# Kernel optimization log

Measured on AMD Instinct MI355X. Metric: run time of the kernel, lower is better.

The kernel has to match this reference:

```python
import jax, jax.numpy as jnp
import numpy as np

N = 20000
E = 320000
IN_DIM = 128
HID = 64
HEADS = 8
OUT_DIM = 128
NEG_SLOPE = 0.2  # PyG GATConv default leaky_relu slope


def _glorot(key, shape):
    fan_in = shape[0] if len(shape) > 1 else shape[-1]
    return jax.random.normal(key, shape, dtype=jnp.float32) / jnp.sqrt(jnp.float32(fan_in))


def setup_inputs() -> dict:
    key = jax.random.key(0)
    ks = jax.random.split(key, 16)
    x = jax.random.normal(ks[0], (N, IN_DIM), dtype=jnp.float32)
    edge_index = jax.random.randint(ks[1], (2, E), 0, N, dtype=jnp.int32)
    HC = HEADS * HID
    return {
        "x": x,
        "edge_index": edge_index,
        # layer 1: in -> heads*hid (concat)
        "W1": _glorot(ks[2], (IN_DIM, HC)),
        "a_src1": _glorot(ks[3], (HEADS, HID)),
        "a_dst1": _glorot(ks[4], (HEADS, HID)),
        "b1": jnp.zeros((HC,), jnp.float32),
        # layer 2: heads*hid -> heads*hid (concat)
        "W2": _glorot(ks[5], (HC, HC)),
        "a_src2": _glorot(ks[6], (HEADS, HID)),
        "a_dst2": _glorot(ks[7], (HEADS, HID)),
        "b2": jnp.zeros((HC,), jnp.float32),
        # layer 3: heads*hid -> out, heads=1, concat=False
        "W3": _glorot(ks[8], (HC, OUT_DIM)),
        "a_src3": _glorot(ks[9], (1, OUT_DIM)),
        "a_dst3": _glorot(ks[10], (1, OUT_DIM)),
        "b3": jnp.zeros((OUT_DIM,), jnp.float32),
    }


def _gat_layer(x, src, dst, W, a_src, a_dst, b, heads, concat):
    # x: [N, F_in] -> h: [N, H, C]
    n = x.shape[0]
    h = (x @ W).reshape(n, heads, -1)
    # per-node attention half-logits: [N, H]
    al_src = jnp.sum(h * a_src[None], axis=-1)
    al_dst = jnp.sum(h * a_dst[None], axis=-1)
    # per-edge logits with leaky relu: [E, H]
    e = jax.nn.leaky_relu(al_src[src] + al_dst[dst], NEG_SLOPE)
    # segment softmax over incoming edges of each dst node
    emax = jax.ops.segment_max(e, dst, num_segments=n)
    ex = jnp.exp(e - emax[dst])
    den = jax.ops.segment_sum(ex, dst, num_segments=n)
    alpha = ex / (den[dst] + 1e-16)
    # weighted scatter-aggregate of source features: [E, H, C] -> [N, H, C]
    out = jax.ops.segment_sum(h[src] * alpha[:, :, None], dst, num_segments=n)
    out = out.reshape(n, -1) if concat else out.mean(axis=1)
    return out + b


def reference(x, edge_index, W1, a_src1, a_dst1, b1, W2, a_src2, a_dst2, b2,
              W3, a_src3, a_dst3, b3):
    # PyG GATConv adds self-loops by default
    loops = jnp.arange(N, dtype=edge_index.dtype)
    src = jnp.concatenate([edge_index[0], loops])
    dst = jnp.concatenate([edge_index[1], loops])
    # eval mode: dropout is identity
    h = _gat_layer(x, src, dst, W1, a_src1, a_dst1, b1, HEADS, True)
    h = jax.nn.elu(h)
    h = _gat_layer(h, src, dst, W2, a_src2, a_dst2, b2, HEADS, True)
    h = jax.nn.elu(h)
    out = _gat_layer(h, src, dst, W3, a_src3, a_dst3, b3, 1, False)
    return out
```

## Files before the change

### kernel.cpp

```cpp
#include <hip/hip_runtime.h>
#include <math.h>

#define NN 20000
#define EE 320000
#define ETOT 340000
#define NHEADS 8
#define HID 64
#define HCV 512
#define IND 128
#define OUTD 128
#define NEG_SLOPE 0.2f
#define LOG2E 1.4426950408889634f

typedef __attribute__((ext_vector_type(8))) _Float16 half8;
typedef __attribute__((ext_vector_type(4))) _Float16 half4;
typedef __attribute__((ext_vector_type(4))) float floatx4;

#define S1 (IND * HCV)
#define S2 (HCV * HCV)
#define S3 (HCV * OUTD)
#define XTOT (NN * IND)

#define NT1 64
#define NT2 320
#define NT_TOT 384
#define XB 2500
__global__ __launch_bounds__(256) void prep_kernel(const float* __restrict__ W1,
                                                   const float* __restrict__ W2,
                                                   const float* __restrict__ W3,
                                                   const float* __restrict__ x,
                                                   _Float16* __restrict__ T1,
                                                   _Float16* __restrict__ T2,
                                                   _Float16* __restrict__ T3,
                                                   _Float16* __restrict__ xh,
                                                   int* __restrict__ cnt) {
    int b = blockIdx.x;
    int tid = threadIdx.x;
    if (b < NT_TOT) {
        __shared__ _Float16 tile[32][34];
        const float* W; _Float16* T; int K, N, tb;
        if (b < NT1)      { W = W1; T = T1; K = IND; N = HCV;  tb = b; }
        else if (b < NT2) { W = W2; T = T2; K = HCV; N = HCV;  tb = b - NT1; }
        else              { W = W3; T = T3; K = HCV; N = OUTD; tb = b - NT2; }
        int ntn = N >> 5;
        int k0 = (tb / ntn) * 32, n0 = (tb % ntn) * 32;
        int tx = tid & 31, ty0 = tid >> 5;
        #pragma unroll
        for (int i = 0; i < 4; i++) {
            int ty = ty0 + 8 * i;
            tile[ty][tx] = (_Float16)W[(size_t)(k0 + ty) * N + n0 + tx];
        }
        __syncthreads();
        #pragma unroll
        for (int i = 0; i < 4; i++) {
            int ty = ty0 + 8 * i;
            T[(size_t)(n0 + ty) * K + k0 + tx] = tile[tx][ty];
        }
    } else if (b < NT_TOT + XB) {
        int idx = (b - NT_TOT) * 256 + tid;
        int j = idx * 4;
        float4 v = *(const float4*)&x[j];
        half4 o;
        o[0] = (_Float16)v.x; o[1] = (_Float16)v.y;
        o[2] = (_Float16)v.z; o[3] = (_Float16)v.w;
        *(half4*)&xh[j] = o;
    } else {
        int idx = (b - NT_TOT - XB) * 256 + tid;
        if (idx < NN) cnt[idx] = 0;
    }
}


__global__ void count_kernel(const int* __restrict__ ei, int* __restrict__ cnt) {
    int i = blockIdx.x * blockDim.x + threadIdx.x;
    if (i >= ETOT) return;
    int v = (i < EE) ? ei[EE + i] : (i - EE);
    atomicAdd(&cnt[v], 1);
}

#define SCH 20
__global__ __launch_bounds__(1024) void scan_kernel(const int* __restrict__ cnt,
                                                    int* __restrict__ row_ptr,
                                                    int* __restrict__ cursor) {
    __shared__ int wtot[16];
    __shared__ int woff[16];
    int t = threadIdx.x;
    int lane = t & 63;
    int wid = t >> 6;
    int base = t * SCH;
    int vals[SCH];
    int s = 0;
    #pragma unroll
    for (int i = 0; i < SCH; i++) {
        int idx = base + i;
        int v = (idx < NN) ? cnt[idx] : 0;
        vals[i] = v;
        s += v;
    }
    int incl = s;
    #pragma unroll
    for (int off = 1; off < 64; off <<= 1) {
        int u = __shfl_up(incl, off);
        if (lane >= off) incl += u;
    }
    int excl = incl - s;
    if (lane == 63) wtot[wid] = incl;
    __syncthreads();
    if (t == 0) {
        int run = 0;
        #pragma unroll
        for (int j = 0; j < 16; j++) { woff[j] = run; run += wtot[j]; }
        row_ptr[NN] = run;
    }
    __syncthreads();
    int run = woff[wid] + excl;
    #pragma unroll
    for (int i = 0; i < SCH; i++) {
        int idx = base + i;
        if (idx < NN) { row_ptr[idx] = run; cursor[idx] = run; run += vals[i]; }
    }
}

__global__ void fill_kernel(const int* __restrict__ ei, int* __restrict__ cursor,
                            int* __restrict__ csr_src) {
    int i = blockIdx.x * blockDim.x + threadIdx.x;
    if (i >= ETOT) return;
    int u, v;
    if (i < EE) { u = ei[i]; v = ei[EE + i]; }
    else        { u = i - EE; v = i - EE; }
    int pos = atomicAdd(&cursor[v], 1);
    csr_src[pos] = u;
}

#define LDK 40
__global__ __launch_bounds__(512) void gemm_al(const _Float16* __restrict__ A,
                                               const _Float16* __restrict__ Bt,
                                               _Float16* __restrict__ C16,
                                               const float* __restrict__ a_src,
                                               const float* __restrict__ a_dst,
                                               float* __restrict__ als2,
                                               float* __restrict__ ald2,
                                               int M, int K) {
    __shared__ _Float16 sA[128 * LDK];
    __shared__ _Float16 sB[128 * LDK];
    __shared__ float psum_s[4][128];
    __shared__ float psum_d[4][128];
    int tid = threadIdx.x;
    int lane = tid & 63;
    int wid = tid >> 6;
    int wv_m = wid >> 2;
    int wv_n = wid & 3;
    int m0 = blockIdx.x * 128, n0 = blockIdx.y * 128;
    int quad = lane >> 4;
    int l15 = lane & 15;
    int arow = tid >> 2;
    int ac4 = tid & 3;

    floatx4 acc[4][2] = {};

    for (int k0 = 0; k0 < K; k0 += 32) {
        {
            int gm = m0 + arow;
            int4 va;
            if (gm < M) va = *(const int4*)&A[(size_t)gm * K + k0 + ac4 * 8];
            else        va = make_int4(0, 0, 0, 0);
            *(int4*)&sA[arow * LDK + ac4 * 8] = va;
            int gn = n0 + arow;
            int4 vb = *(const int4*)&Bt[(size_t)gn * K + k0 + ac4 * 8];
            *(int4*)&sB[arow * LDK + ac4 * 8] = vb;
        }
        __syncthreads();
        half8 a[4], b[2];
        #pragma unroll
        for (int i = 0; i < 4; i++)
            a[i] = *(const half8*)&sA[(wv_m * 64 + i * 16 + l15) * LDK + quad * 8];
        #pragma unroll
        for (int j = 0; j < 2; j++)
            b[j] = *(const half8*)&sB[(wv_n * 32 + j * 16 + l15) * LDK + quad * 8];
        #pragma unroll
        for (int i = 0; i < 4; i++)
            #pragma unroll
            for (int j = 0; j < 2; j++)
                acc[i][j] = __builtin_amdgcn_mfma_f32_16x16x32_f16(a[i], b[j], acc[i][j], 0, 0, 0);
        __syncthreads();
    }
    #pragma unroll
    for (int i = 0; i < 4; i++) {
        #pragma unroll
        for (int r = 0; r < 4; r++) {
            int gm = m0 + wv_m * 64 + i * 16 + quad * 4 + r;
            if (gm < M) {
                #pragma unroll
                for (int j = 0; j < 2; j++)
                    C16[(size_t)gm * HCV + n0 + wv_n * 32 + j * 16 + l15] = (_Float16)acc[i][j][r];
            }
        }
    }
    int h0 = n0 >> 6;
    int hh = h0 + (wv_n >> 1);
    float as_v[2], ad_v[2];
    #pragma unroll
    for (int j = 0; j < 2; j++) {
        int dim = (wv_n * 32 + j * 16 + l15) & 63;
        as_v[j] = a_src[hh * HID + dim] * LOG2E;
        ad_v[j] = a_dst[hh * HID + dim] * LOG2E;
    }
    #pragma unroll
    for (int i = 0; i < 4; i++) {
        #pragma unroll
        for (int r = 0; r < 4; r++) {
            float ps = acc[i][0][r] * as_v[0] + acc[i][1][r] * as_v[1];
            float pd = acc[i][0][r] * ad_v[0] + acc[i][1][r] * ad_v[1];
            #pragma unroll
            for (int off = 1; off <= 8; off <<= 1) {
                ps += __shfl_xor(ps, off);
                pd += __shfl_xor(pd, off);
            }
            if (l15 == 0) {
                int row = wv_m * 64 + i * 16 + quad * 4 + r;
                psum_s[wv_n][row] = ps;
                psum_d[wv_n][row] = pd;
            }
        }
    }
    __syncthreads();
    if (tid < 128) {
        int gm = m0 + tid;
        if (gm < M) {
            als2[(size_t)h0 * NN + gm]       = psum_s[0][tid] + psum_s[1][tid];
            als2[(size_t)(h0 + 1) * NN + gm] = psum_s[2][tid] + psum_s[3][tid];
            ald2[(size_t)h0 * NN + gm]       = psum_d[0][tid] + psum_d[1][tid];
            ald2[(size_t)(h0 + 1) * NN + gm] = psum_d[2][tid] + psum_d[3][tid];
        }
    }
}

__global__ __launch_bounds__(256) void gemm3(const _Float16* __restrict__ A,
                                             const _Float16* __restrict__ Bt,
                                             _Float16* __restrict__ C16,
                                             const float* __restrict__ a_src,
                                             const float* __restrict__ a_dst,
                                             float* __restrict__ als,
                                             float* __restrict__ ald,
                                             int M, int K) {
    __shared__ _Float16 sA[64 * LDK];
    __shared__ _Float16 sB[128 * LDK];
    __shared__ float psum_s[4][64];
    __shared__ float psum_d[4][64];
    int tid = threadIdx.x;
    int lane = tid & 63;
    int wv = tid >> 6;
    int m0 = blockIdx.x * 64;
    int quad = lane >> 4;
    int l15 = lane & 15;
    int arow = tid >> 2;
    int ac4 = tid & 3;

    floatx4 acc[4][2] = {};

    for (int k0 = 0; k0 < K; k0 += 32) {
        {
            int gm = m0 + arow;
            int4 va;
            if (gm < M && arow < 64) va = *(const int4*)&A[(size_t)gm * K + k0 + ac4 * 8];
            else                     va = make_int4(0, 0, 0, 0);
            if (arow < 64) *(int4*)&sA[arow * LDK + ac4 * 8] = va;
            #pragma unroll
            for (int r = 0; r < 2; r++) {
                int gn = arow + r * 64;
                int4 vb = *(const int4*)&Bt[(size_t)gn * K + k0 + ac4 * 8];
                *(int4*)&sB[(arow + r * 64) * LDK + ac4 * 8] = vb;
            }
        }
        __syncthreads();
        half8 a[4], b[2];
        #pragma unroll
        for (int i = 0; i < 4; i++)
            a[i] = *(const half8*)&sA[(i * 16 + l15) * LDK + quad * 8];
        #pragma unroll
        for (int j = 0; j < 2; j++)
            b[j] = *(const half8*)&sB[(wv * 32 + j * 16 + l15) * LDK + quad * 8];
        #pragma unroll
        for (int i = 0; i < 4; i++)
            #pragma unroll
            for (int j = 0; j < 2; j++)
                acc[i][j] = __builtin_amdgcn_mfma_f32_16x16x32_f16(a[i], b[j], acc[i][j], 0, 0, 0);
        __syncthreads();
    }
    #pragma unroll
    for (int i = 0; i < 4; i++) {
        #pragma unroll
        for (int r = 0; r < 4; r++) {
            int gm = m0 + i * 16 + quad * 4 + r;
            if (gm < M) {
                #pragma unroll
                for (int j = 0; j < 2; j++)
                    C16[(size_t)gm * OUTD + wv * 32 + j * 16 + l15] = (_Float16)acc[i][j][r];
            }
        }
    }
    float as_v[2], ad_v[2];
    #pragma unroll
    for (int j = 0; j < 2; j++) {
        as_v[j] = a_src[wv * 32 + j * 16 + l15] * LOG2E;
        ad_v[j] = a_dst[wv * 32 + j * 16 + l15] * LOG2E;
    }
    #pragma unroll
    for (int i = 0; i < 4; i++) {
        #pragma unroll
        for (int r = 0; r < 4; r++) {
            float ps = acc[i][0][r] * as_v[0] + acc[i][1][r] * as_v[1];
            float pd = acc[i][0][r] * ad_v[0] + acc[i][1][r] * ad_v[1];
            #pragma unroll
            for (int off = 1; off <= 8; off <<= 1) {
                ps += __shfl_xor(ps, off);
                pd += __shfl_xor(pd, off);
            }
            if (l15 == 0) {
                int row = i * 16 + quad * 4 + r;
                psum_s[wv][row] = ps;
                psum_d[wv][row] = pd;
            }
        }
    }
    __syncthreads();
    if (tid < 64) {
        int gm = m0 + tid;
        if (gm < M) {
            als[gm] = psum_s[0][tid] + psum_s[1][tid] + psum_s[2][tid] + psum_s[3][tid];
            ald[gm] = psum_d[0][tid] + psum_d[1][tid] + psum_d[2][tid] + psum_d[3][tid];
        }
    }
}

__global__ __launch_bounds__(256) void gather_kernel(const _Float16* __restrict__ h,
                                                     const int* __restrict__ row_ptr,
                                                     const int* __restrict__ csr_src,
                                                     const float* __restrict__ als2,
                                                     const float* __restrict__ ald2,
                                                     const float* __restrict__ bias,
                                                     _Float16* __restrict__ gout) {
    int tid = threadIdx.x;
    int lane = tid & 63;
    int wid = tid >> 6;
    int bid = blockIdx.x;
    int hd = bid & 7;
    int dl = lane & 7;
    int es = (lane >> 3) & 1;
    int sub = lane >> 4;
    int v = (bid >> 3) * 16 + wid * 4 + sub;
    if (v >= NN) return;
    const float* asl = als2 + (size_t)hd * NN;
    float adst = ald2[(size_t)hd * NN + v];
    int s0 = row_ptr[v], s1 = row_ptr[v + 1];
    int mid = (s0 + s1 + 1) >> 1;
    int jb = es ? mid : s0;
    int je = es ? s1 : mid;
    const _Float16* hh = h + hd * HID + dl * 8;
    float acc[8] = {};
    float l = 0.f;
    int j = jb;
    for (; j + 4 <= je; j += 4) {
        int u[4]; float p[4]; half8 xv[4];
        #pragma unroll
        for (int e = 0; e < 4; e++) u[e] = csr_src[j + e];
        #pragma unroll
        for (int e = 0; e < 4; e++) xv[e] = *(const half8*)&hh[(size_t)u[e] * HCV];
        #pragma unroll
        for (int e = 0; e < 4; e++) {
            float t = asl[u[e]] + adst;
            t = (t > 0.f) ? t : NEG_SLOPE * t;
            p[e] = exp2f(fminf(t, 115.f));
        }
        #pragma unroll
        for (int e = 0; e < 4; e++) {
            l += p[e];
            #pragma unroll
            for (int k = 0; k < 8; k++)
                acc[k] = fmaf(p[e], (float)xv[e][k], acc[k]);
        }
    }
    for (; j < je; j++) {
        int u0 = csr_src[j];
        half8 x0 = *(const half8*)&hh[(size_t)u0 * HCV];
        float t0 = asl[u0] + adst;
        t0 = (t0 > 0.f) ? t0 : NEG_SLOPE * t0;
        float p0 = exp2f(fminf(t0, 115.f));
        l += p0;
        #pragma unroll
        for (int k = 0; k < 8; k++)
            acc[k] = fmaf(p0, (float)x0[k], acc[k]);
    }
    l += __shfl_xor(l, 8);
    #pragma unroll
    for (int k = 0; k < 8; k++)
        acc[k] += __shfl_xor(acc[k], 8);
    if (es == 0) {
        float inv = 1.f / (l + 1e-16f);
        half8 hv;
        #pragma unroll
        for (int k = 0; k < 8; k++) {
            float o = fmaf(acc[k], inv, bias[hd * HID + dl * 8 + k]);
            o = (o > 0.f) ? o : (__expf(o) - 1.f);
            hv[k] = (_Float16)o;
        }
        half8* dst = (half8*)&gout[(size_t)v * HCV + hd * HID + dl * 8];
        __builtin_nontemporal_store(hv, dst);
    }
}

__global__ __launch_bounds__(256) void gather3_kernel(const _Float16* __restrict__ h,
                                                      const int* __restrict__ row_ptr,
                                                      const int* __restrict__ csr_src,
                                                      const float* __restrict__ als,
                                                      const float* __restrict__ ald,
                                                      const float* __restrict__ bias,
                                                      float* __restrict__ out) {
    int tid = threadIdx.x;
    int lane = tid & 63;
    int wid = tid >> 6;
    int bid = blockIdx.x;
    int dh = bid & 1;
    int dl = lane & 7;
    int es = (lane >> 3) & 1;
    int sub = lane >> 4;
    int l16 = lane & 15;
    int v = (bid >> 1) * 16 + wid * 4 + sub;
    if (v >= NN) return;
    float adst = ald[v];
    int s0 = row_ptr[v], s1 = row_ptr[v + 1];
    float m = -INFINITY;
    for (int j = s0 + l16; j < s1; j += 16) {
        int u = csr_src[j];
        float t = als[u] + adst;
        t = (t > 0.f) ? t : NEG_SLOPE * t;
        m = fmaxf(m, t);
    }
    #pragma unroll
    for (int off = 1; off <= 8; off <<= 1)
        m = fmaxf(m, __shfl_xor(m, off));
    int mid = (s0 + s1 + 1) >> 1;
    int jb = es ? mid : s0;
    int je = es ? s1 : mid;
    const _Float16* hh = h + dh * 64 + dl * 8;
    float acc[8] = {};
    float l = 0.f;
    int j = jb;
    for (; j + 2 <= je; j += 2) {
        int u0 = csr_src[j], u1 = csr_src[j + 1];
        float t0 = als[u0] + adst;
        float t1 = als[u1] + adst;
        t0 = (t0 > 0.f) ? t0 : NEG_SLOPE * t0;
        t1 = (t1 > 0.f) ? t1 : NEG_SLOPE * t1;
        float p0 = exp2f(t0 - m);
        float p1 = exp2f(t1 - m);
        half8 x0 = *(const half8*)&hh[(size_t)u0 * OUTD];
        half8 x1 = *(const half8*)&hh[(size_t)u1 * OUTD];
        l += p0 + p1;
        #pragma unroll
        for (int k = 0; k < 8; k++) {
            acc[k] = fmaf(p0, (float)x0[k], acc[k]);
            acc[k] = fmaf(p1, (float)x1[k], acc[k]);
        }
    }
    if (j < je) {
        int u0 = csr_src[j];
        float t0 = als[u0] + adst;
        t0 = (t0 > 0.f) ? t0 : NEG_SLOPE * t0;
        float p0 = exp2f(t0 - m);
        half8 x0 = *(const half8*)&hh[(size_t)u0 * OUTD];
        l += p0;
        #pragma unroll
        for (int k = 0; k < 8; k++)
            acc[k] = fmaf(p0, (float)x0[k], acc[k]);
    }
    l += __shfl_xor(l, 8);
    #pragma unroll
    for (int k = 0; k < 8; k++)
        acc[k] += __shfl_xor(acc[k], 8);
    if (es == 0) {
        float inv = 1.f / (l + 1e-16f);
        float4 o0, o1;
        o0.x = fmaf(acc[0], inv, bias[dh * 64 + dl * 8 + 0]);
        o0.y = fmaf(acc[1], inv, bias[dh * 64 + dl * 8 + 1]);
        o0.z = fmaf(acc[2], inv, bias[dh * 64 + dl * 8 + 2]);
        o0.w = fmaf(acc[3], inv, bias[dh * 64 + dl * 8 + 3]);
        o1.x = fmaf(acc[4], inv, bias[dh * 64 + dl * 8 + 4]);
        o1.y = fmaf(acc[5], inv, bias[dh * 64 + dl * 8 + 5]);
        o1.z = fmaf(acc[6], inv, bias[dh * 64 + dl * 8 + 6]);
        o1.w = fmaf(acc[7], inv, bias[dh * 64 + dl * 8 + 7]);
        size_t base = (size_t)v * OUTD + dh * 64 + dl * 8;
        *(float4*)&out[base] = o0;
        *(float4*)&out[base + 4] = o1;
    }
}


extern "C" void kernel_launch(void* const* d_in, const int* in_sizes, int n_in,
                              void* d_out, int out_size, void* d_ws, size_t ws_size,
                              hipStream_t stream) {
    const float* x     = (const float*)d_in[0];
    const int*   ei    = (const int*)d_in[1];
    const float* W1    = (const float*)d_in[2];
    const float* as1   = (const float*)d_in[3];
    const float* ad1   = (const float*)d_in[4];
    const float* b1    = (const float*)d_in[5];
    const float* W2    = (const float*)d_in[6];
    const float* as2   = (const float*)d_in[7];
    const float* ad2   = (const float*)d_in[8];
    const float* b2    = (const float*)d_in[9];
    const float* W3    = (const float*)d_in[10];
    const float* as3   = (const float*)d_in[11];
    const float* ad3   = (const float*)d_in[12];
    const float* b3    = (const float*)d_in[13];
    float* out = (float*)d_out;

    size_t off = 0;
    auto carve = [&](size_t bytes) {
        void* p = (char*)d_ws + off;
        off += (bytes + 255) & ~(size_t)255;
        return p;
    };
    int* row_ptr   = (int*)carve((NN + 1) * sizeof(int));
    int* cursor    = (int*)carve(NN * sizeof(int));
    int* csr_src   = (int*)carve(ETOT * sizeof(int));
    _Float16* xh   = (_Float16*)carve((size_t)NN * IND * sizeof(_Float16));
    _Float16* h1   = (_Float16*)carve((size_t)NN * HCV * sizeof(_Float16));
    _Float16* gact = (_Float16*)carve((size_t)NN * HCV * sizeof(_Float16));
    _Float16* hf16 = (_Float16*)carve((size_t)NN * HCV * sizeof(_Float16));
    _Float16* h3   = (_Float16*)carve((size_t)NN * OUTD * sizeof(_Float16));
    float* als     = (float*)carve((size_t)NN * NHEADS * sizeof(float));
    float* ald     = (float*)carve((size_t)NN * NHEADS * sizeof(float));
    _Float16* W1T  = (_Float16*)carve((size_t)S1 * sizeof(_Float16));
    _Float16* W2T  = (_Float16*)carve((size_t)S2 * sizeof(_Float16));
    _Float16* W3T  = (_Float16*)carve((size_t)S3 * sizeof(_Float16));
    _Float16* gact2 = h1;
    (void)ws_size; (void)n_in; (void)in_sizes; (void)out_size;

    dim3 blk(256);

    int prep_blocks = NT_TOT + XB + (NN + 255) / 256;
    prep_kernel<<<prep_blocks, blk, 0, stream>>>(W1, W2, W3, x, W1T, W2T, W3T, xh, cursor);

    count_kernel<<<(ETOT + 255) / 256, blk, 0, stream>>>(ei, cursor);
    scan_kernel<<<1, 1024, 0, stream>>>(cursor, row_ptr, cursor);
    fill_kernel<<<(ETOT + 255) / 256, blk, 0, stream>>>(ei, cursor, csr_src);

    int mt64 = (NN + 63) / 64;
    int mt128 = (NN + 127) / 128;
    int nb4 = (NN + 15) / 16;

    gemm_al<<<dim3(mt128, HCV / 128), dim3(512), 0, stream>>>(xh, W1T, h1, as1, ad1, als, ald, NN, IND);
    gather_kernel<<<dim3(nb4 * 8), blk, 0, stream>>>(h1, row_ptr, csr_src, als, ald, b1, gact);

    gemm_al<<<dim3(mt128, HCV / 128), dim3(512), 0, stream>>>(gact, W2T, hf16, as2, ad2, als, ald, NN, HCV);
    gather_kernel<<<dim3(nb4 * 8), blk, 0, stream>>>(hf16, row_ptr, csr_src, als, ald, b2, gact2);

    gemm3<<<dim3(mt64, 1), blk, 0, stream>>>(gact2, W3T, h3, as3, ad3, als, ald, NN, HCV);
    gather3_kernel<<<dim3(nb4 * 2), blk, 0, stream>>>(h3, row_ptr, csr_src, als, ald, b3, out);
}
```

Before: 310.1 us.

## Use direct global-to-LDS loads with XOR swizzle and deepen aggregation unrolling

The 128x128 GEMM now fills shared memory with global_load_lds (direct global-to-LDS DMA) instead of going through registers, and uses an XOR-swizzled unpadded layout to avoid LDS bank conflicts. The intent is to cut register staging and VGPR pressure in the tile load. Separately, the multi-head aggregation loop gains an 8-edge unrolled stage and the final-layer aggregation goes from 2-wide to 4-wide unrolling, putting more gather loads in flight. The risks are higher register use and a skipped zero-fill: out-of-range A rows now leave stale LDS data, though those rows are never stored.

```diff
diff --git a/kernel.cpp b/kernel.cpp
--- a/kernel.cpp
+++ b/kernel.cpp
@@ -132,7 +132,7 @@
     csr_src[pos] = u;
 }
 
-#define LDK 40
+#define BK 32
 __global__ __launch_bounds__(512) void gemm_al(const _Float16* __restrict__ A,
                                                const _Float16* __restrict__ Bt,
                                                _Float16* __restrict__ C16,
@@ -141,8 +141,8 @@
                                                float* __restrict__ als2,
                                                float* __restrict__ ald2,
                                                int M, int K) {
-    __shared__ _Float16 sA[128 * LDK];
-    __shared__ _Float16 sB[128 * LDK];
+    __shared__ _Float16 sA[128 * BK];
+    __shared__ _Float16 sB[128 * BK];
     __shared__ float psum_s[4][128];
     __shared__ float psum_d[4][128];
     int tid = threadIdx.x;
@@ -153,30 +153,48 @@
     int m0 = blockIdx.x * 128, n0 = blockIdx.y * 128;
     int quad = lane >> 4;
     int l15 = lane & 15;
-    int arow = tid >> 2;
-    int ac4 = tid & 3;
+
+    int phys = wid * 1024 + lane * 16;
+    int logical = phys ^ (((phys >> 7) & 3) << 4);
+    int lrow = logical >> 6;
+    int lcol = (logical >> 4) & 3;
+    int gmA = m0 + lrow;
+    const _Float16* gA = A + (size_t)gmA * K + lcol * 8;
+    const _Float16* gB = Bt + (size_t)(n0 + lrow) * K + lcol * 8;
+    bool aok = (gmA < M);
+    _Float16* lA = sA + wid * 512;
+    _Float16* lB = sB + wid * 512;
+
+    int ra[4], rb[2];
+    #pragma unroll
+    for (int i = 0; i < 4; i++) {
+        int lb = (wv_m * 64 + i * 16 + l15) * 64 + quad * 16;
+        ra[i] = lb ^ (((lb >> 7) & 3) << 4);
+    }
+    #pragma unroll
+    for (int j = 0; j < 2; j++) {
+        int lb = (wv_n * 32 + j * 16 + l15) * 64 + quad * 16;
+        rb[j] = lb ^ (((lb >> 7) & 3) << 4);
+    }
 
     floatx4 acc[4][2] = {};
 
-    for (int k0 = 0; k0 < K; k0 += 32) {
-        {
-            int gm = m0 + arow;
-            int4 va;
-            if (gm < M) va = *(const int4*)&A[(size_t)gm * K + k0 + ac4 * 8];
-            else        va = make_int4(0, 0, 0, 0);
-            *(int4*)&sA[arow * LDK + ac4 * 8] = va;
-            int gn = n0 + arow;
-            int4 vb = *(const int4*)&Bt[(size_t)gn * K + k0 + ac4 * 8];
-            *(int4*)&sB[arow * LDK + ac4 * 8] = vb;
-        }
+    for (int k0 = 0; k0 < K; k0 += BK) {
+        if (aok)
+            __builtin_amdgcn_global_load_lds(
+                (const __attribute__((address_space(1))) void*)(gA + k0),
+                (__attribute__((address_space(3))) void*)lA, 16, 0, 0);
+        __builtin_amdgcn_global_load_lds(
+            (const __attribute__((address_space(1))) void*)(gB + k0),
+            (__attribute__((address_space(3))) void*)lB, 16, 0, 0);
         __syncthreads();
         half8 a[4], b[2];
         #pragma unroll
         for (int i = 0; i < 4; i++)
-            a[i] = *(const half8*)&sA[(wv_m * 64 + i * 16 + l15) * LDK + quad * 8];
+            a[i] = *(const half8*)((const char*)sA + ra[i]);
         #pragma unroll
         for (int j = 0; j < 2; j++)
-            b[j] = *(const half8*)&sB[(wv_n * 32 + j * 16 + l15) * LDK + quad * 8];
+            b[j] = *(const half8*)((const char*)sB + rb[j]);
         #pragma unroll
         for (int i = 0; i < 4; i++)
             #pragma unroll
@@ -235,6 +253,7 @@
     }
 }
 
+#define LDK 40
 __global__ __launch_bounds__(256) void gemm3(const _Float16* __restrict__ A,
                                              const _Float16* __restrict__ Bt,
                                              _Float16* __restrict__ C16,
@@ -360,6 +379,26 @@
     float acc[8] = {};
     float l = 0.f;
     int j = jb;
+    for (; j + 8 <= je; j += 8) {
+        int u[8]; float p[8]; half8 xv[8];
+        #pragma unroll
+        for (int e = 0; e < 8; e++) u[e] = csr_src[j + e];
+        #pragma unroll
+        for (int e = 0; e < 8; e++) xv[e] = *(const half8*)&hh[(size_t)u[e] * HCV];
+        #pragma unroll
+        for (int e = 0; e < 8; e++) {
+            float t = asl[u[e]] + adst;
+            t = (t > 0.f) ? t : NEG_SLOPE * t;
+            p[e] = exp2f(fminf(t, 115.f));
+        }
+        #pragma unroll
+        for (int e = 0; e < 8; e++) {
+            l += p[e];
+            #pragma unroll
+            for (int k = 0; k < 8; k++)
+                acc[k] = fmaf(p[e], (float)xv[e][k], acc[k]);
+        }
+    }
     for (; j + 4 <= je; j += 4) {
         int u[4]; float p[4]; half8 xv[4];
         #pragma unroll
@@ -446,24 +485,27 @@
     float acc[8] = {};
     float l = 0.f;
     int j = jb;
-    for (; j + 2 <= je; j += 2) {
-        int u0 = csr_src[j], u1 = csr_src[j + 1];
-        float t0 = als[u0] + adst;
-        float t1 = als[u1] + adst;
-        t0 = (t0 > 0.f) ? t0 : NEG_SLOPE * t0;
-        t1 = (t1 > 0.f) ? t1 : NEG_SLOPE * t1;
-        float p0 = exp2f(t0 - m);
-        float p1 = exp2f(t1 - m);
-        half8 x0 = *(const half8*)&hh[(size_t)u0 * OUTD];
-        half8 x1 = *(const half8*)&hh[(size_t)u1 * OUTD];
-        l += p0 + p1;
-        #pragma unroll
-        for (int k = 0; k < 8; k++) {
-            acc[k] = fmaf(p0, (float)x0[k], acc[k]);
-            acc[k] = fmaf(p1, (float)x1[k], acc[k]);
-        }
-    }
-    if (j < je) {
+    for (; j + 4 <= je; j += 4) {
+        int u[4]; float p[4]; half8 xv[4];
+        #pragma unroll
+        for (int e = 0; e < 4; e++) u[e] = csr_src[j + e];
+        #pragma unroll
+        for (int e = 0; e < 4; e++) xv[e] = *(const half8*)&hh[(size_t)u[e] * OUTD];
+        #pragma unroll
+        for (int e = 0; e < 4; e++) {
+            float t = als[u[e]] + adst;
+            t = (t > 0.f) ? t : NEG_SLOPE * t;
+            p[e] = exp2f(t - m);
+        }
+        #pragma unroll
+        for (int e = 0; e < 4; e++) {
+            l += p[e];
+            #pragma unroll
+            for (int k = 0; k < 8; k++)
+                acc[k] = fmaf(p[e], (float)xv[e][k], acc[k]);
+        }
+    }
+    for (; j < je; j++) {
         int u0 = csr_src[j];
         float t0 = als[u0] + adst;
         t0 = (t0 > 0.f) ? t0 : NEG_SLOPE * t0;
```

After: 333.0 us. 1.07x slower.
